# Kernel tuning notes

Measured on AMD Instinct MI355X. Metric: run time of the kernel, lower is better.

The kernel has to match this reference:

```python
import jax, jax.numpy as jnp
import numpy as np

FEATURE_DIM = 63
DIM = 64
B, N = 1024, 256


def setup_inputs() -> dict:
    key = jax.random.key(0)
    ks = jax.random.split(key, 10)
    # padded batched dense adjacency [B, N, N] (includes self-loops + supernode edges in real data)
    adj = (jax.random.uniform(ks[0], (B, N, N), dtype=jnp.float32) < 0.05).astype(jnp.float32)
    adj = adj + jnp.eye(N, dtype=jnp.float32)[None]  # self loops as in process()
    vec = jax.random.normal(ks[1], (B, N, FEATURE_DIM), dtype=jnp.float32)
    s1 = 1.0 / np.sqrt(FEATURE_DIM)
    s2 = 1.0 / np.sqrt(DIM)
    return {
        "adj": adj,
        "vec": vec,
        "w1_rel": jax.random.normal(ks[2], (FEATURE_DIM, DIM), dtype=jnp.float32) * s1,
        "w1_root": jax.random.normal(ks[3], (FEATURE_DIM, DIM), dtype=jnp.float32) * s1,
        "b1": jnp.zeros((DIM,), dtype=jnp.float32),
        "w2_rel": jax.random.normal(ks[4], (DIM, DIM), dtype=jnp.float32) * s2,
        "w2_root": jax.random.normal(ks[5], (DIM, DIM), dtype=jnp.float32) * s2,
        "b2": jnp.zeros((DIM,), dtype=jnp.float32),
        "wf": jax.random.normal(ks[6], (DIM, 2), dtype=jnp.float32) * s2,
        "bf": jnp.zeros((2,), dtype=jnp.float32),
    }


def dense_graph_conv(adj, x, w_rel, w_root, b):
    # PyG DenseGraphConv: lin_rel(adj @ x) + lin_root(x)
    agg = jnp.einsum('bij,bjf->bif', adj, x)  # [B,N,F] neighbor aggregation
    return agg @ w_rel + x @ w_root + b


def reference(adj, vec, w1_rel, w1_root, b1, w2_rel, w2_root, b2, wf, bf):
    x = jax.nn.relu(dense_graph_conv(adj, vec, w1_rel, w1_root, b1))  # [B,N,dim]
    y = jax.nn.relu(dense_graph_conv(adj, x, w2_rel, w2_root, b2))    # [B,N,dim]
    # readout at node 0 (virtual supernode), then linear head -> [B,2]
    return (x[:, 0] + y[:, 0]) @ wf + bf
```

## Files before the change

### kernel.cpp

```cpp
#include <hip/hip_runtime.h>


#define NB 1024
#define NN 256
#define FD 63
#define DM 64
#define MAXP 32
#define VT 264
#define W72 72

using short8 = __attribute__((ext_vector_type(8))) short;
using f32x4  = __attribute__((ext_vector_type(4))) float;

__device__ __forceinline__ short f2bf(float f) {
    unsigned u = __builtin_bit_cast(unsigned, f);
    unsigned r = (u + 0x7FFFu + ((u >> 16) & 1u)) >> 16;
    return (short)r;
}
__device__ __forceinline__ float bf2f(short s) {
    return __builtin_bit_cast(float, ((unsigned)(unsigned short)s) << 16);
}

__launch_bounds__(256, 2)
__global__ void gnn_node0_mfma(const float* __restrict__ adj,
                               const float* __restrict__ vec,
                               const float* __restrict__ w1_rel,
                               const float* __restrict__ w1_root,
                               const float* __restrict__ b1,
                               const float* __restrict__ w2_rel,
                               const float* __restrict__ w2_root,
                               const float* __restrict__ b2,
                               const float* __restrict__ wf,
                               const float* __restrict__ bf,
                               float* __restrict__ out)
{
    __shared__ __align__(16) short s_vecT[DM * VT];
    __shared__ __align__(16) short s_adj[MAXP * VT];
    __shared__ __align__(16) short s_aggb[MAXP * W72];
    __shared__ __align__(16) short s_w1relT[DM * W72];
    __shared__ __align__(16) short s_w1rootT[DM * W72];
    __shared__ float s_accp[4][DM];
    __shared__ float s_rA[DM], s_rB[DM], s_r[DM];
    __shared__ float s_pA[4][DM];
    __shared__ float s_a0[MAXP];
    __shared__ int   s_nbr[MAXP];
    __shared__ int   s_cnt, s_p0;

    const int b    = blockIdx.x;
    const int t    = threadIdx.x;
    const int lane = t & 63;
    const int q    = t >> 6;
    const int lr   = lane & 15;
    const int lg   = lane >> 4;
    const int mt   = q & 1;
    const int ntb  = (q >> 1) * 2;
    const float* adj_b = adj + (size_t)b * NN * NN;
    const float* vec_b = vec + (size_t)b * NN * FD;

    if (t == 0) { s_cnt = 0; s_p0 = 0; }
    if (t < MAXP) { s_a0[t] = 0.f; s_nbr[t] = 0; }
    __syncthreads();

    {
        float a = adj_b[t];
        if (a != 0.f) {
            int idx = atomicAdd(&s_cnt, 1);
            if (idx < MAXP) { s_nbr[idx] = t; s_a0[idx] = a; if (t == 0) s_p0 = idx; }
        }
    }
    for (int i = t; i < FD * DM; i += 256) {
        const int k = i >> 6, d = i & 63;
        s_w1relT[d * W72 + k]  = f2bf(w1_rel[i]);
        s_w1rootT[d * W72 + k] = f2bf(w1_root[i]);
    }
    if (t < DM) { s_w1relT[t * W72 + 63] = 0; s_w1rootT[t * W72 + 63] = 0; }
    #pragma unroll 4
    for (int r = 0; r < 64; ++r) {
        const int k = r * 4 + q;
        if (lane < FD) s_vecT[lane * VT + k] = f2bf(vec_b[k * FD + lane]);
    }
    for (int i = t; i < VT; i += 256) s_vecT[63 * VT + i] = 0;
    __syncthreads();

    const int cnt = min(s_cnt, MAXP);
    const int p0  = s_p0;

    for (int p = 0; p < MAXP; ++p) {
        if (p < cnt) {
            const int j = s_nbr[p];
            s_adj[p * VT + t] = f2bf(adj_b[j * NN + t]);
        } else {
            s_adj[p * VT + t] = 0;
        }
    }
    __syncthreads();

    {
        f32x4 acc0 = {0.f, 0.f, 0.f, 0.f};
        f32x4 acc1 = {0.f, 0.f, 0.f, 0.f};
        const short* arow = &s_adj[(lr + 16 * mt) * VT];
        const short* brow0 = &s_vecT[(lr + 16 * ntb) * VT];
        const short* brow1 = &s_vecT[(lr + 16 * ntb + 16) * VT];
        #pragma unroll
        for (int ks = 0; ks < 8; ++ks) {
            const int ko = ks * 32 + lg * 8;
            const short8 av = *reinterpret_cast<const short8*>(arow + ko);
            const short8 b0 = *reinterpret_cast<const short8*>(brow0 + ko);
            const short8 b1v = *reinterpret_cast<const short8*>(brow1 + ko);
            acc0 = __builtin_amdgcn_mfma_f32_16x16x32_bf16(av, b0, acc0, 0, 0, 0);
            acc1 = __builtin_amdgcn_mfma_f32_16x16x32_bf16(av, b1v, acc1, 0, 0, 0);
        }
        #pragma unroll
        for (int r = 0; r < 4; ++r) {
            const int row = lg * 4 + r + 16 * mt;
            s_aggb[row * W72 + lr + 16 * ntb]      = f2bf(acc0[r]);
            s_aggb[row * W72 + lr + 16 * ntb + 16] = f2bf(acc1[r]);
        }
    }
    __syncthreads();

    {
        f32x4 acc0 = {0.f, 0.f, 0.f, 0.f};
        f32x4 acc1 = {0.f, 0.f, 0.f, 0.f};
        const int prow = lr + 16 * mt;
        const int jsel = s_nbr[prow];
        const short* aggrow = &s_aggb[prow * W72];
        const short* bR0 = &s_w1relT[(lr + 16 * ntb) * W72];
        const short* bR1 = &s_w1relT[(lr + 16 * ntb + 16) * W72];
        const short* bO0 = &s_w1rootT[(lr + 16 * ntb) * W72];
        const short* bO1 = &s_w1rootT[(lr + 16 * ntb + 16) * W72];
        #pragma unroll
        for (int ks = 0; ks < 2; ++ks) {
            const int ko = ks * 32 + lg * 8;
            const short8 aA = *reinterpret_cast<const short8*>(aggrow + ko);
            short8 aV;
            #pragma unroll
            for (int u = 0; u < 8; ++u)
                aV[u] = s_vecT[(ko + u) * VT + jsel];
            const short8 vR0 = *reinterpret_cast<const short8*>(bR0 + ko);
            const short8 vR1 = *reinterpret_cast<const short8*>(bR1 + ko);
            const short8 vO0 = *reinterpret_cast<const short8*>(bO0 + ko);
            const short8 vO1 = *reinterpret_cast<const short8*>(bO1 + ko);
            acc0 = __builtin_amdgcn_mfma_f32_16x16x32_bf16(aA, vR0, acc0, 0, 0, 0);
            acc0 = __builtin_amdgcn_mfma_f32_16x16x32_bf16(aV, vO0, acc0, 0, 0, 0);
            acc1 = __builtin_amdgcn_mfma_f32_16x16x32_bf16(aA, vR1, acc1, 0, 0, 0);
            acc1 = __builtin_amdgcn_mfma_f32_16x16x32_bf16(aV, vO1, acc1, 0, 0, 0);
        }
        const int c0 = lr + 16 * ntb, c1 = c0 + 16;
        const float bc0 = b1[c0], bc1 = b1[c1];
        float aY0 = 0.f, aY1 = 0.f;
        #pragma unroll
        for (int r = 0; r < 4; ++r) {
            const int row = lg * 4 + r + 16 * mt;
            const float a0 = s_a0[row];
            const float x0v = fmaxf(acc0[r] + bc0, 0.f);
            const float x1v = fmaxf(acc1[r] + bc1, 0.f);
            aY0 += a0 * x0v;
            aY1 += a0 * x1v;
            if (row == p0) { s_rB[c0] = x0v; s_rB[c1] = x1v; }
        }
        aY0 += __shfl_xor(aY0, 16); aY0 += __shfl_xor(aY0, 32);
        aY1 += __shfl_xor(aY1, 16); aY1 += __shfl_xor(aY1, 32);
        if (lg == 0) { s_accp[q][c0] = aY0; s_accp[q][c1] = aY1; }
    }
    __syncthreads();

    if (q == 0) {
        const int qp = 2 * (lane >> 5);
        s_rA[lane] = s_accp[qp][lane] + s_accp[qp + 1][lane];
    }
    __syncthreads();

    {
        float p = 0.f;
        const int f0 = q * 16;
        #pragma unroll
        for (int ff2 = 0; ff2 < 16; ++ff2) {
            const int ff = f0 + ff2;
            p += s_rA[ff] * w2_rel[ff * DM + lane]
               + s_rB[ff] * w2_root[ff * DM + lane];
        }
        s_pA[q][lane] = p;
    }
    __syncthreads();
    if (t < DM) {
        const float y = fmaxf(s_pA[0][t] + s_pA[1][t] + s_pA[2][t] + s_pA[3][t] + b2[t], 0.f);
        s_r[t] = s_rB[t] + y;
    }
    __syncthreads();
    if (t < 2) {
        float acc = bf[t];
        #pragma unroll
        for (int d = 0; d < DM; ++d) acc += s_r[d] * wf[d * 2 + t];
        out[b * 2 + t] = acc;
    }
}

extern "C" void kernel_launch(void* const* d_in, const int* in_sizes, int n_in,
                              void* d_out, int out_size, void* d_ws, size_t ws_size,
                              hipStream_t stream) {
    const float* adj     = (const float*)d_in[0];
    const float* vec     = (const float*)d_in[1];
    const float* w1_rel  = (const float*)d_in[2];
    const float* w1_root = (const float*)d_in[3];
    const float* b1      = (const float*)d_in[4];
    const float* w2_rel  = (const float*)d_in[5];
    const float* w2_root = (const float*)d_in[6];
    const float* b2      = (const float*)d_in[7];
    const float* wf      = (const float*)d_in[8];
    const float* bf      = (const float*)d_in[9];
    float* out = (float*)d_out;

    gnn_node0_mfma<<<NB, 256, 0, stream>>>(adj, vec, w1_rel, w1_root, b1,
                                           w2_rel, w2_root, b2, wf, bf, out);
}
```

Before: 380.2 us.

## Load adjacency rows directly into MFMA fragments and prepack W1 fragments in a pre-kernel

Neighbor adjacency rows are now loaded straight from global memory into register MFMA A-fragments, which removes the shared s_adj staging buffer and one barrier. W1 weights are converted to bf16 and packed into MFMA fragment order once by a small pre-kernel writing to workspace, so each block no longer transposes them. The vec transpose now uses vectorized 16-byte LDS stores. Shared memory use drops, so launch bounds are raised to 3 blocks per CU. The cost is one extra launch and higher register pressure from holding 16 float4 adjacency values per thread.

Result: faster. 357.5 us (-6.0%).

```diff
diff --git a/kernel.cpp b/kernel.cpp
--- a/kernel.cpp
+++ b/kernel.cpp
@@ -14,34 +14,50 @@
 
 __device__ __forceinline__ short f2bf(float f) {
     unsigned u = __builtin_bit_cast(unsigned, f);
-    unsigned r = (u + 0x7FFFu + ((u >> 16) & 1u)) >> 16;
-    return (short)r;
-}
-__device__ __forceinline__ float bf2f(short s) {
-    return __builtin_bit_cast(float, ((unsigned)(unsigned short)s) << 16);
-}
-
-__launch_bounds__(256, 2)
+    return (short)((u + 0x7FFFu + ((u >> 16) & 1u)) >> 16);
+}
+
+__global__ void k0_w1frag(const float* __restrict__ w1_rel,
+                          const float* __restrict__ w1_root,
+                          short8* __restrict__ outR,
+                          short8* __restrict__ outO)
+{
+    const int fi = blockIdx.x * blockDim.x + threadIdx.x;
+    if (fi >= 512) return;
+    const int lane = fi & 63, ksn = fi >> 6;
+    const int ks = ksn & 1, nt = ksn >> 1;
+    const int n  = (lane & 15) + 16 * nt;
+    const int kb = ks * 32 + (lane >> 4) * 8;
+    short8 r, o;
+    #pragma unroll
+    for (int u = 0; u < 8; ++u) {
+        const int k = kb + u;
+        const bool ok = (k < FD);
+        r[u] = ok ? f2bf(w1_rel[k * DM + n])  : (short)0;
+        o[u] = ok ? f2bf(w1_root[k * DM + n]) : (short)0;
+    }
+    outR[fi] = r;
+    outO[fi] = o;
+}
+
+__launch_bounds__(256, 3)
 __global__ void gnn_node0_mfma(const float* __restrict__ adj,
                                const float* __restrict__ vec,
-                               const float* __restrict__ w1_rel,
-                               const float* __restrict__ w1_root,
                                const float* __restrict__ b1,
                                const float* __restrict__ w2_rel,
                                const float* __restrict__ w2_root,
                                const float* __restrict__ b2,
                                const float* __restrict__ wf,
                                const float* __restrict__ bf,
+                               const short8* __restrict__ w1fR,
+                               const short8* __restrict__ w1fO,
                                float* __restrict__ out)
 {
     __shared__ __align__(16) short s_vecT[DM * VT];
-    __shared__ __align__(16) short s_adj[MAXP * VT];
     __shared__ __align__(16) short s_aggb[MAXP * W72];
-    __shared__ __align__(16) short s_w1relT[DM * W72];
-    __shared__ __align__(16) short s_w1rootT[DM * W72];
     __shared__ float s_accp[4][DM];
+    __shared__ float s_pA[4][DM];
     __shared__ float s_rA[DM], s_rB[DM], s_r[DM];
-    __shared__ float s_pA[4][DM];
     __shared__ float s_a0[MAXP];
     __shared__ int   s_nbr[MAXP];
     __shared__ int   s_cnt, s_p0;
@@ -68,47 +84,60 @@
             if (idx < MAXP) { s_nbr[idx] = t; s_a0[idx] = a; if (t == 0) s_p0 = idx; }
         }
     }
-    for (int i = t; i < FD * DM; i += 256) {
-        const int k = i >> 6, d = i & 63;
-        s_w1relT[d * W72 + k]  = f2bf(w1_rel[i]);
-        s_w1rootT[d * W72 + k] = f2bf(w1_root[i]);
-    }
-    if (t < DM) { s_w1relT[t * W72 + 63] = 0; s_w1rootT[t * W72 + 63] = 0; }
-    #pragma unroll 4
-    for (int r = 0; r < 64; ++r) {
-        const int k = r * 4 + q;
-        if (lane < FD) s_vecT[lane * VT + k] = f2bf(vec_b[k * FD + lane]);
-    }
-    for (int i = t; i < VT; i += 256) s_vecT[63 * VT + i] = 0;
-    __syncthreads();
-
-    const int cnt = min(s_cnt, MAXP);
-    const int p0  = s_p0;
-
-    for (int p = 0; p < MAXP; ++p) {
-        if (p < cnt) {
-            const int j = s_nbr[p];
-            s_adj[p * VT + t] = f2bf(adj_b[j * NN + t]);
-        } else {
-            s_adj[p * VT + t] = 0;
-        }
-    }
-    __syncthreads();
+    __syncthreads();
+
+    const int jmine = s_nbr[lr + 16 * mt];
+    f32x4 araw[16];
+    {
+        const float* rp = adj_b + (size_t)jmine * NN + lg * 8;
+        #pragma unroll
+        for (int ks = 0; ks < 8; ++ks) {
+            araw[2 * ks]     = *reinterpret_cast<const f32x4*>(rp + ks * 32);
+            araw[2 * ks + 1] = *reinterpret_cast<const f32x4*>(rp + ks * 32 + 4);
+        }
+    }
+
+    if (lane < FD) {
+        const int kb0 = q * 64;
+        #pragma unroll 2
+        for (int r0 = 0; r0 < 64; r0 += 8) {
+            float v[8];
+            #pragma unroll
+            for (int u = 0; u < 8; ++u) v[u] = vec_b[(kb0 + r0 + u) * FD + lane];
+            short8 sv;
+            #pragma unroll
+            for (int u = 0; u < 8; ++u) sv[u] = f2bf(v[u]);
+            *reinterpret_cast<short8*>(&s_vecT[lane * VT + kb0 + r0]) = sv;
+        }
+    }
+    for (int i = t; i < NN; i += 256) s_vecT[63 * VT + i] = 0;
+
+    short8 afrag[8];
+    #pragma unroll
+    for (int ks = 0; ks < 8; ++ks) {
+        short8 s;
+        #pragma unroll
+        for (int u = 0; u < 4; ++u) {
+            s[u]     = f2bf(araw[2 * ks][u]);
+            s[4 + u] = f2bf(araw[2 * ks + 1][u]);
+        }
+        afrag[ks] = s;
+    }
+    __syncthreads();
+
+    const int p0 = s_p0;
 
     {
         f32x4 acc0 = {0.f, 0.f, 0.f, 0.f};
         f32x4 acc1 = {0.f, 0.f, 0.f, 0.f};
-        const short* arow = &s_adj[(lr + 16 * mt) * VT];
-        const short* brow0 = &s_vecT[(lr + 16 * ntb) * VT];
-        const short* brow1 = &s_vecT[(lr + 16 * ntb + 16) * VT];
+        const short* b0p = &s_vecT[(lr + 16 * ntb) * VT + lg * 8];
+        const short* b1p = &s_vecT[(lr + 16 * ntb + 16) * VT + lg * 8];
         #pragma unroll
         for (int ks = 0; ks < 8; ++ks) {
-            const int ko = ks * 32 + lg * 8;
-            const short8 av = *reinterpret_cast<const short8*>(arow + ko);
-            const short8 b0 = *reinterpret_cast<const short8*>(brow0 + ko);
-            const short8 b1v = *reinterpret_cast<const short8*>(brow1 + ko);
-            acc0 = __builtin_amdgcn_mfma_f32_16x16x32_bf16(av, b0, acc0, 0, 0, 0);
-            acc1 = __builtin_amdgcn_mfma_f32_16x16x32_bf16(av, b1v, acc1, 0, 0, 0);
+            const short8 bf0 = *reinterpret_cast<const short8*>(b0p + ks * 32);
+            const short8 bf1 = *reinterpret_cast<const short8*>(b1p + ks * 32);
+            acc0 = __builtin_amdgcn_mfma_f32_16x16x32_bf16(afrag[ks], bf0, acc0, 0, 0, 0);
+            acc1 = __builtin_amdgcn_mfma_f32_16x16x32_bf16(afrag[ks], bf1, acc1, 0, 0, 0);
         }
         #pragma unroll
         for (int r = 0; r < 4; ++r) {
@@ -124,23 +153,19 @@
         f32x4 acc1 = {0.f, 0.f, 0.f, 0.f};
         const int prow = lr + 16 * mt;
         const int jsel = s_nbr[prow];
-        const short* aggrow = &s_aggb[prow * W72];
-        const short* bR0 = &s_w1relT[(lr + 16 * ntb) * W72];
-        const short* bR1 = &s_w1relT[(lr + 16 * ntb + 16) * W72];
-        const short* bO0 = &s_w1rootT[(lr + 16 * ntb) * W72];
-        const short* bO1 = &s_w1rootT[(lr + 16 * ntb + 16) * W72];
+        const short* aggrow = &s_aggb[prow * W72 + lg * 8];
         #pragma unroll
         for (int ks = 0; ks < 2; ++ks) {
             const int ko = ks * 32 + lg * 8;
-            const short8 aA = *reinterpret_cast<const short8*>(aggrow + ko);
+            const short8 aA = *reinterpret_cast<const short8*>(aggrow + ks * 32);
             short8 aV;
             #pragma unroll
             for (int u = 0; u < 8; ++u)
                 aV[u] = s_vecT[(ko + u) * VT + jsel];
-            const short8 vR0 = *reinterpret_cast<const short8*>(bR0 + ko);
-            const short8 vR1 = *reinterpret_cast<const short8*>(bR1 + ko);
-            const short8 vO0 = *reinterpret_cast<const short8*>(bO0 + ko);
-            const short8 vO1 = *reinterpret_cast<const short8*>(bO1 + ko);
+            const short8 vR0 = w1fR[((ntb    ) * 2 + ks) * 64 + lane];
+            const short8 vR1 = w1fR[((ntb + 1) * 2 + ks) * 64 + lane];
+            const short8 vO0 = w1fO[((ntb    ) * 2 + ks) * 64 + lane];
+            const short8 vO1 = w1fO[((ntb + 1) * 2 + ks) * 64 + lane];
             acc0 = __builtin_amdgcn_mfma_f32_16x16x32_bf16(aA, vR0, acc0, 0, 0, 0);
             acc0 = __builtin_amdgcn_mfma_f32_16x16x32_bf16(aV, vO0, acc0, 0, 0, 0);
             acc1 = __builtin_amdgcn_mfma_f32_16x16x32_bf16(aA, vR1, acc1, 0, 0, 0);
@@ -211,6 +236,10 @@
     const float* bf      = (const float*)d_in[9];
     float* out = (float*)d_out;
 
-    gnn_node0_mfma<<<NB, 256, 0, stream>>>(adj, vec, w1_rel, w1_root, b1,
-                                           w2_rel, w2_root, b2, wf, bf, out);
-}
+    short8* wsR = (short8*)d_ws;
+    short8* wsO = wsR + 512;
+
+    k0_w1frag<<<2, 256, 0, stream>>>(w1_rel, w1_root, wsR, wsO);
+    gnn_node0_mfma<<<NB, 256, 0, stream>>>(adj, vec, b1, w2_rel, w2_root,
+                                           b2, wf, bf, wsR, wsO, out);
+}
```
